# Kernel optimization log

Hardware: AMD Instinct MI355X
Metric: run time of the kernel (lower is better)

## Reference

```python
import jax, jax.numpy as jnp
import numpy as np
import math
from jax import lax

IMG = 1024
STRIDES = (4, 8, 16, 32, 64)
RATIOS = (0.5, 1.0, 2.0)
PRE_NMS = 1000      # pre_nms_top_n['testing'] per level
POST_NMS = 1000     # post_nms_top_n['testing']
NMS_T = 0.7
MIN_SIZE = 1e-3
SCORE_T = 0.0
BBOX_CLAMP = math.log(1000.0 / 16.0)  # torchvision BoxCoder clamp
LEVEL_SIZES = tuple(((IMG // s) ** 2) * len(RATIOS) for s in STRIDES)  # (196608,49152,12288,3072,768)
A_TOTAL = sum(LEVEL_SIZES)
N_IMG = 16


def _make_anchors():
    ratios = np.asarray(RATIOS, dtype=np.float64)
    h_r = np.sqrt(ratios)
    w_r = 1.0 / h_r
    out = []
    for lvl, s in enumerate(STRIDES):
        size = 32.0 * (2 ** lvl)
        ws, hs = w_r * size, h_r * size
        base = np.stack([-ws / 2, -hs / 2, ws / 2, hs / 2], axis=1)  # [A,4]
        g = IMG // s
        coords = np.arange(g, dtype=np.float64) * s
        sx, sy = np.meshgrid(coords, coords)  # [g,g], row = H
        shifts = np.stack([sx, sy, sx, sy], axis=-1).reshape(-1, 1, 4)  # [g*g,1,4] in (H,W,A) order
        out.append((shifts + base[None]).reshape(-1, 4))
    return np.concatenate(out, 0).astype(np.float32)


def setup_inputs() -> dict:
    key = jax.random.key(0)
    k1, k2 = jax.random.split(key)
    objectness = jax.random.normal(k1, (N_IMG, A_TOTAL), dtype=jnp.float32)
    deltas = jax.random.normal(k2, (N_IMG, A_TOTAL, 4), dtype=jnp.float32) * 0.1
    anchors = jnp.asarray(_make_anchors())
    return {"objectness": objectness, "deltas": deltas, "anchors": anchors}


def _decode(deltas, anchors):
    # torchvision BoxCoder.decode with weights (1,1,1,1); deltas [N,A,4], anchors [A,4]
    wa = anchors[:, 2] - anchors[:, 0]
    ha = anchors[:, 3] - anchors[:, 1]
    cxa = anchors[:, 0] + 0.5 * wa
    cya = anchors[:, 1] + 0.5 * ha
    dx, dy, dw, dh = (deltas[..., 0], deltas[..., 1], deltas[..., 2], deltas[..., 3])
    dw = jnp.minimum(dw, BBOX_CLAMP)
    dh = jnp.minimum(dh, BBOX_CLAMP)
    cx = dx * wa + cxa
    cy = dy * ha + cya
    w = jnp.exp(dw) * wa
    h = jnp.exp(dh) * ha
    return jnp.stack([cx - 0.5 * w, cy - 0.5 * h, cx + 0.5 * w, cy + 0.5 * h], axis=-1)


def _nms_image(boxes, scores, lvl, valid):
    # batched_nms via per-level coordinate offset, then greedy NMS over score-sorted boxes.
    max_c = jnp.max(boxes)
    off = lvl.astype(boxes.dtype) * (max_c + 1.0)
    b_off = boxes + off[:, None]
    s = jnp.where(valid, scores, -1.0)
    order = jnp.argsort(-s)
    b = b_off[order]          # [K,4] offset boxes, score-descending
    bo = boxes[order]
    so = scores[order]
    vo = valid[order]
    K = b.shape[0]
    areas = (b[:, 2] - b[:, 0]) * (b[:, 3] - b[:, 1])
    idx = jnp.arange(K)

    def body(keep, xs):
        i, bi, vi = xs
        lt = jnp.maximum(bi[:2], b[:, :2])
        rb = jnp.minimum(bi[2:], b[:, 2:])
        wh = jnp.clip(rb - lt, 0.0)
        inter = wh[:, 0] * wh[:, 1]
        ai = (bi[2] - bi[0]) * (bi[3] - bi[1])
        union = ai + areas - inter
        iou = jnp.where(union > 0, inter / union, 0.0)
        suppressed = jnp.any(keep & (idx < i) & (iou > NMS_T))
        return keep.at[i].set(vi & ~suppressed), None

    keep, _ = lax.scan(body, jnp.zeros((K,), bool), (idx, b, vo))
    # compact kept entries (already score-ordered) into POST_NMS slots, pad with zeros
    pos = jnp.cumsum(keep) - 1
    slot = jnp.where(keep & (pos < POST_NMS), pos, POST_NMS)
    out_b = jnp.zeros((POST_NMS + 1, 4), boxes.dtype).at[slot].set(bo)[:POST_NMS]
    out_s = jnp.zeros((POST_NMS + 1,), boxes.dtype).at[slot].set(so)[:POST_NMS]
    return out_b, out_s


def reference(objectness, deltas, anchors):
    N = objectness.shape[0]
    proposals = _decode(deltas, anchors)  # [N,A,4]
    # per-level top-k (pre-NMS)
    idxs = []
    offset = 0
    for n in LEVEL_SIZES:
        k = min(PRE_NMS, n)
        _, ti = lax.top_k(objectness[:, offset:offset + n], k)
        idxs.append(ti + offset)
        offset += n
    top_idx = jnp.concatenate(idxs, axis=1)  # [N,K]
    obj = jnp.take_along_axis(objectness, top_idx, axis=1)
    props = jnp.take_along_axis(proposals, top_idx[..., None], axis=1)
    lvl_full = jnp.asarray(np.repeat(np.arange(len(LEVEL_SIZES)), LEVEL_SIZES))
    lvl = lvl_full[top_idx]
    scores = jax.nn.sigmoid(obj)
    # clip to image
    x = jnp.clip(props[..., 0::2], 0.0, float(IMG))
    y = jnp.clip(props[..., 1::2], 0.0, float(IMG))
    boxes = jnp.stack([x[..., 0], y[..., 0], x[..., 1], y[..., 1]], axis=-1)
    # remove small boxes + score threshold (as validity mask)
    w = boxes[..., 2] - boxes[..., 0]
    h = boxes[..., 3] - boxes[..., 1]
    valid = (w >= MIN_SIZE) & (h >= MIN_SIZE) & (scores >= SCORE_T)
    out_boxes, out_scores = jax.vmap(_nms_image)(boxes, scores, lvl, valid)
    return out_boxes, out_scores
```

## Files before the change

kernel.cpp:

```cpp
#include <hip/hip_runtime.h>
#include <stdint.h>

#define NIMG 16
#define ATOT 261888
#define TOTC 4768
#define POSTN 1000
#define ROWQ 75
#define EQCAP 8192
#define SCAP 1088
#define BPRE 24
#define DM 0.7000000178813934326171875

__device__ __forceinline__ unsigned sortable_u32(float f) {
  unsigned b = __float_as_uint(f);
  return (b & 0x80000000u) ? ~b : (b | 0x80000000u);
}

__device__ __forceinline__ float exp_xla(float x) {
  float xc = fminf(x, 88.72283935546875f);
  xc = fmaxf(xc, -87.33654022216796875f);
  float n = floorf(fmaf(xc, 1.44269504088896341f, 0.5f));
  float r = fmaf(n, -0.693359375f, xc);
  r = fmaf(n, 2.12194440e-4f, r);
  float y = 1.9875691500e-4f;
  y = fmaf(y, r, 1.3981999507e-3f);
  y = fmaf(y, r, 8.3334519073e-3f);
  y = fmaf(y, r, 4.1665795894e-2f);
  y = fmaf(y, r, 1.6666665459e-1f);
  y = fmaf(y, r, 5.0000001201e-1f);
  float r2 = r * r;
  y = fmaf(y, r2, r);
  y = y + 1.0f;
  return ldexpf(y, (int)n);
}

__device__ __forceinline__ float sigmoid_ref(float x) {
#pragma clang fp contract(off)
  float e = exp_xla(-x);
  return 1.0f / (1.0f + e);
}

__device__ __forceinline__ void chunk_map4k(int c, int& lvl, int& start, int& cnt) {
  if (c < 48)      { lvl = 0; start = c * 4096;        cnt = 4096; }
  else if (c < 60) { lvl = 1; start = (c - 48) * 4096; cnt = 4096; }
  else if (c < 63) { lvl = 2; start = (c - 60) * 4096; cnt = 4096; }
  else             { lvl = 3; start = 0;               cnt = 3072; }
}
__constant__ int d_LO[5] = {0, 196608, 245760, 258048, 261120};
__constant__ int d_CO[5] = {0, 1000, 2000, 3000, 4000};

__global__ void __launch_bounds__(256) k_hist(const float* __restrict__ obj,
                                              unsigned* __restrict__ hist) {
  int img = blockIdx.x >> 6, c = blockIdx.x & 63;
  int lvl, start, cnt;
  chunk_map4k(c, lvl, start, cnt);
  const float4* p4 = (const float4*)(obj + (size_t)img * ATOT + d_LO[lvl] + start);
  __shared__ unsigned h[256];
  h[threadIdx.x] = 0;
  __syncthreads();
  int nv = cnt >> 2;
  for (int i = threadIdx.x; i < nv; i += 256) {
    float4 v = p4[i];
    atomicAdd(&h[sortable_u32(v.x) >> 24], 1u);
    atomicAdd(&h[sortable_u32(v.y) >> 24], 1u);
    atomicAdd(&h[sortable_u32(v.z) >> 24], 1u);
    atomicAdd(&h[sortable_u32(v.w) >> 24], 1u);
  }
  __syncthreads();
  unsigned* gh = hist + (img * 4 + lvl) * 256;
  if (h[threadIdx.x]) atomicAdd(&gh[threadIdx.x], h[threadIdx.x]);
}

__global__ void __launch_bounds__(64) k_thresh(const unsigned* __restrict__ hist,
                                               unsigned* __restrict__ thr) {
  int il = blockIdx.x;
  if (threadIdx.x != 0) return;
  const unsigned* h = hist + il * 256;
  unsigned krem = 1000, cum = 0;
  int d = 255;
  for (; d > 0; --d) {
    if (cum + h[d] >= krem) break;
    cum += h[d];
  }
  thr[il * 2] = (unsigned)d;
  thr[il * 2 + 1] = krem - cum;
}

__global__ void __launch_bounds__(256) k_emit(const float* __restrict__ obj,
                                              const unsigned* __restrict__ thr,
                                              int* __restrict__ cand,
                                              int* __restrict__ eqbuf,
                                              unsigned* __restrict__ cnt) {
  int img = blockIdx.x / 65, c = blockIdx.x % 65;
  if (c == 64) {
    for (int i = threadIdx.x; i < 768; i += 256)
      cand[img * TOTC + d_CO[4] + i] = d_LO[4] + i;
    return;
  }
  int lvl, start, cntn;
  chunk_map4k(c, lvl, start, cntn);
  int il = img * 4 + lvl;
  unsigned d0 = thr[il * 2];
  int gbase = d_LO[lvl] + start;
  const float4* p4 = (const float4*)(obj + (size_t)img * ATOT + gbase);
  int nv = cntn >> 2;
  int cbase = img * TOTC + d_CO[lvl];

  __shared__ int gts[SCAP], eqs[SCAP];
  __shared__ int nGt, nEq, gtBase, eqBase;
  if (threadIdx.x == 0) { nGt = 0; nEq = 0; }
  __syncthreads();

  float4 v[4];
  int ni = 0;
#pragma unroll
  for (int k = 0; k < 4; ++k) {
    int i = threadIdx.x + k * 256;
    if (i < nv) { v[k] = p4[i]; ni = k + 1; }
  }
#pragma unroll
  for (int k = 0; k < 4; ++k) {
    if (k >= ni) break;
    float vv[4] = {v[k].x, v[k].y, v[k].z, v[k].w};
#pragma unroll
    for (int c4 = 0; c4 < 4; ++c4) {
      unsigned u = sortable_u32(vv[c4]);
      unsigned d = u >> 24;
      if (d >= d0) {
        int gidx = gbase + (threadIdx.x + k * 256) * 4 + c4;
        if (d > d0) {
          int p = atomicAdd(&nGt, 1);
          if (p < SCAP) gts[p] = gidx;
          else { int s = (int)atomicAdd(&cnt[il * 2], 1u); cand[cbase + s] = gidx; }
        } else {
          int p = atomicAdd(&nEq, 1);
          if (p < SCAP) eqs[p] = gidx;
          else { int e = (int)atomicAdd(&cnt[il * 2 + 1], 1u); if (e < EQCAP) eqbuf[il * EQCAP + e] = gidx; }
        }
      }
    }
  }
  __syncthreads();
  int ng = nGt < SCAP ? nGt : SCAP;
  int ne = nEq < SCAP ? nEq : SCAP;
  if (threadIdx.x == 0) {
    gtBase = (int)atomicAdd(&cnt[il * 2], (unsigned)ng);
    eqBase = (int)atomicAdd(&cnt[il * 2 + 1], (unsigned)ne);
  }
  __syncthreads();
  for (int k = threadIdx.x; k < ng; k += 256) cand[cbase + gtBase + k] = gts[k];
  for (int k = threadIdx.x; k < ne; k += 256) {
    int e = eqBase + k;
    if (e < EQCAP) eqbuf[il * EQCAP + e] = eqs[k];
  }
}

__global__ void __launch_bounds__(256) k_refine(const float* __restrict__ obj,
                                                const unsigned* __restrict__ thr,
                                                const int* __restrict__ eqbuf,
                                                const unsigned* __restrict__ cnt,
                                                int* __restrict__ cand) {
  int il = blockIdx.x;
  int img = il >> 2, lvl = il & 3;
  unsigned pref = thr[il * 2];
  unsigned krem = thr[il * 2 + 1];
  int neq = min((int)cnt[il * 2 + 1], EQCAP);
  int cgt = (int)cnt[il * 2];
  const float* p = obj + (size_t)img * ATOT;
  const int* eq = eqbuf + il * EQCAP;
  int cbase = img * TOTC + d_CO[lvl];
  __shared__ unsigned h[256];
  __shared__ unsigned s_pref, s_krem;
  for (int round = 1; round < 4; ++round) {
    int shift = 24 - 8 * round;
    h[threadIdx.x] = 0;
    __syncthreads();
    for (int e = threadIdx.x; e < neq; e += 256) {
      unsigned u = sortable_u32(p[eq[e]]);
      if ((u >> (shift + 8)) == pref) atomicAdd(&h[(u >> shift) & 255u], 1u);
    }
    __syncthreads();
    if (threadIdx.x == 0) {
      unsigned cum = 0;
      int d = 255;
      for (; d > 0; --d) {
        if (cum + h[d] >= krem) break;
        cum += h[d];
      }
      s_pref = (pref << 8) | (unsigned)d;
      s_krem = krem - cum;
    }
    __syncthreads();
    pref = s_pref;
    krem = s_krem;
    __syncthreads();
  }
  __shared__ int cg2, ce2;
  __shared__ int eqi[1024];
  if (threadIdx.x == 0) { cg2 = 0; ce2 = 0; }
  __syncthreads();
  for (int e = threadIdx.x; e < neq; e += 256) {
    int gidx = eq[e];
    unsigned u = sortable_u32(p[gidx]);
    if (u > pref) {
      int s = atomicAdd(&cg2, 1);
      cand[cbase + cgt + s] = gidx;
    } else if (u == pref) {
      int s2 = atomicAdd(&ce2, 1);
      if (s2 < 1024) eqi[s2] = gidx;
    }
  }
  __syncthreads();
  if (threadIdx.x == 0) {
    int ne = ce2 < 1024 ? ce2 : 1024;
    int base = cgt + cg2;
    for (int r = 0; r < (int)krem; ++r) {
      int besti = -1, bestv = 0x7fffffff;
      for (int e2 = 0; e2 < ne; ++e2) {
        int v = eqi[e2];
        if (v >= 0 && v < bestv) { bestv = v; besti = e2; }
      }
      if (besti < 0) break;
      eqi[besti] = -1;
      cand[cbase + base + r] = bestv;
    }
  }
}

__global__ void __launch_bounds__(1024) k_lvlsort(const float* __restrict__ obj,
                                                  int* __restrict__ cand) {
  const int KL[5] = {1000, 1000, 1000, 1000, 768};
  const int CO[5] = {0, 1000, 2000, 3000, 4000};
  int img = blockIdx.x / 5, lvl = blockIdx.x % 5;
  int k = KL[lvl];
  int cbase = img * TOTC + CO[lvl];
  int tid = threadIdx.x;
  __shared__ unsigned long long sh[1024];
  unsigned long long key = 0ull;
  if (tid < k) {
    int idx = cand[cbase + tid];
    unsigned u = sortable_u32(obj[(size_t)img * ATOT + idx]);
    key = ((unsigned long long)u << 32) | (unsigned)(0xFFFFFFFFu - (unsigned)idx);
  }
  sh[tid] = key;
  __syncthreads();
  for (int kk = 2; kk <= 1024; kk <<= 1)
    for (int j = kk >> 1; j > 0; j >>= 1) {
      int ixj = tid ^ j;
      if (ixj > tid) {
        unsigned long long a = sh[tid], b = sh[ixj];
        bool up2 = ((tid & kk) == 0);
        if ((a < b) == up2) { sh[tid] = b; sh[ixj] = a; }
      }
      __syncthreads();
    }
  if (tid < k) {
    unsigned low = (unsigned)(sh[tid] & 0xFFFFFFFFull);
    cand[cbase + tid] = (int)(0xFFFFFFFFu - low);
  }
}

__global__ void __launch_bounds__(256) k_decode(const float* __restrict__ obj,
                                                const float* __restrict__ del,
                                                const float* __restrict__ anc,
                                                const int* __restrict__ cand,
                                                float* __restrict__ boxo,
                                                float* __restrict__ keyf,
                                                unsigned* __restrict__ skey,
                                                unsigned* __restrict__ maxcb) {
#pragma clang fp contract(off)
  int img = blockIdx.x;
  int c = blockIdx.y * 256 + threadIdx.x;
  float m = 0.0f;
  if (c < TOTC) {
    int a = cand[img * TOTC + c];
    float o = obj[(size_t)img * ATOT + a];
    float s = sigmoid_ref(o);
    const float* ap = anc + (size_t)a * 4;
    float a0 = ap[0], a1 = ap[1], a2 = ap[2], a3 = ap[3];
    const float* dp = del + ((size_t)img * ATOT + (size_t)a) * 4;
    float dx = dp[0], dy = dp[1], dw = dp[2], dh = dp[3];
    float wa = a2 - a0, ha = a3 - a1;
    float cxa = a0 + 0.5f * wa, cya = a1 + 0.5f * ha;
    dw = fminf(dw, 4.135166556742356f);
    dh = fminf(dh, 4.135166556742356f);
    float cx = dx * wa + cxa;
    float cy = dy * ha + cya;
    float w = exp_xla(dw) * wa;
    float h = exp_xla(dh) * ha;
    float x1 = cx - 0.5f * w, y1 = cy - 0.5f * h;
    float x2 = cx + 0.5f * w, y2 = cy + 0.5f * h;
    x1 = fminf(fmaxf(x1, 0.0f), 1024.0f);
    x2 = fminf(fmaxf(x2, 0.0f), 1024.0f);
    y1 = fminf(fmaxf(y1, 0.0f), 1024.0f);
    y2 = fminf(fmaxf(y2, 0.0f), 1024.0f);
    float ww = x2 - x1, hh = y2 - y1;
    bool valid = (ww >= 1e-3f) && (hh >= 1e-3f) && (s >= 0.0f);
    float kf = valid ? s : -1.0f;
    float4 bx = make_float4(x1, y1, x2, y2);
    *(float4*)(boxo + (size_t)(img * TOTC + c) * 4) = bx;
    keyf[img * TOTC + c] = kf;
    skey[img * TOTC + c] = sortable_u32(kf);
    m = fmaxf(fmaxf(x1, x2), fmaxf(y1, y2));
  }
  __shared__ float red[256];
  red[threadIdx.x] = m;
  __syncthreads();
  for (int s2 = 128; s2 > 0; s2 >>= 1) {
    if (threadIdx.x < s2) red[threadIdx.x] = fmaxf(red[threadIdx.x], red[threadIdx.x + s2]);
    __syncthreads();
  }
  if (threadIdx.x == 0) atomicMax(&maxcb[img], __float_as_uint(red[0]));
}

__global__ void __launch_bounds__(256) k_rank(const unsigned* __restrict__ skey,
                                              int* __restrict__ ord) {
  int img = blockIdx.x / 19;
  int tile = blockIdx.x % 19;
  __shared__ unsigned long long keys[TOTC];
  const unsigned* sk = skey + img * TOTC;
  for (int k = threadIdx.x; k < TOTC; k += 256)
    keys[k] = ((unsigned long long)sk[k] << 16) | (unsigned)(0xFFFF - k);
  __syncthreads();
  int i = tile * 256 + threadIdx.x;
  if (i >= TOTC) return;
  unsigned long long my = keys[i];
  int cnt = 0;
  int j = 0;
  for (; j + 8 <= TOTC; j += 8) {
#pragma unroll
    for (int u = 0; u < 8; ++u) cnt += (keys[j + u] > my) ? 1 : 0;
  }
  for (; j < TOTC; ++j) cnt += (keys[j] > my) ? 1 : 0;
  ord[img * TOTC + cnt] = i;
}

__global__ void __launch_bounds__(256) k_srec(const float* __restrict__ boxo,
                                              const float* __restrict__ keyf,
                                              const int* __restrict__ ord,
                                              const unsigned* __restrict__ maxcb,
                                              float* __restrict__ srec,
                                              int* __restrict__ rinv,
                                              unsigned long long* __restrict__ validw) {
#pragma clang fp contract(off)
  int img = blockIdx.x;
  int i = blockIdx.y * 256 + threadIdx.x;
  if (i >= TOTC) return;
  int p = ord[img * TOTC + i];
  int lvl = p / 1000;
  if (lvl > 4) lvl = 4;
  float4 b = *(const float4*)(boxo + (size_t)(img * TOTC + p) * 4);
  float maxc = __uint_as_float(maxcb[img]);
  float off = (float)lvl * (maxc + 1.0f);
  float ox1 = b.x + off, oy1 = b.y + off, ox2 = b.z + off, oy2 = b.w + off;
  float area = (ox2 - ox1) * (oy2 - oy1);
  float kf = keyf[img * TOTC + p];
  float* r = srec + (size_t)(img * TOTC + i) * 12;
  r[0] = ox1; r[1] = oy1; r[2] = ox2; r[3] = oy2;
  r[4] = area; r[5] = kf;
  r[6] = b.x; r[7] = b.y; r[8] = b.z; r[9] = b.w;
  r[10] = __int_as_float(lvl); r[11] = 0.0f;
  rinv[img * TOTC + p] = i;
  bool valid = kf > -0.5f;
  unsigned long long vb = __ballot(valid);
  if ((threadIdx.x & 63) == 0 && (i >> 6) < ROWQ) validw[img * ROWQ + (i >> 6)] = vb;
}

__global__ void __launch_bounds__(256) k_iou(const float* __restrict__ srec,
                                             unsigned long long* __restrict__ mat) {
#pragma clang fp contract(off)
  int gb = blockIdx.x;
  int img = gb / 21;
  int g = gb % 21;
  int t, jcg;
  if (g < 6)       { t = 0; jcg = g; }
  else if (g < 11) { t = 1; jcg = g - 6; }
  else if (g < 15) { t = 2; jcg = g - 11; }
  else if (g < 18) { t = 3; jcg = g - 15; }
  else if (g < 20) { t = 4; jcg = g - 18; }
  else             { t = 5; jcg = g - 20; }
  int jcbase = (t + jcg) * 4;

  const int tid = threadIdx.x;
  const int i = t * 256 + tid;
  const float* sb = srec + (size_t)img * TOTC * 12;

  __shared__ float4 s_box[256];
  __shared__ float s_area[256];
  {
    int j = jcbase * 64 + tid;
    const float* r = sb + (size_t)j * 12;
    s_box[tid] = *(const float4*)r;
    s_area[tid] = r[4];
  }

  const float* rr = sb + (size_t)i * 12;
  float4 bb = *(const float4*)rr;
  float ix1 = bb.x, iy1 = bb.y, ix2 = bb.z, iy2 = bb.w;
  float ia = rr[4];
  __syncthreads();

  unsigned long long* rowp = mat + ((size_t)img * TOTC + (size_t)i) * ROWQ;
#pragma unroll
  for (int kk = 0; kk < 4; ++kk) {
    int jc = jcbase + kk;
    unsigned long long bits = 0ull;
    for (int b = 0; b < 64; ++b) {
      float4 jb = s_box[kk * 64 + b];
      float ja = s_area[kk * 64 + b];
      float ltx = fmaxf(ix1, jb.x), lty = fmaxf(iy1, jb.y);
      float rbx = fminf(ix2, jb.z), rby = fminf(iy2, jb.w);
      float w = fmaxf(rbx - ltx, 0.0f), h = fmaxf(rby - lty, 0.0f);
      float inter = w * h;
      float uni = (ia + ja) - inter;
      bool sup = (uni > 0.0f) && ((double)inter >= DM * (double)uni);
      if (sup) bits |= (1ull << b);
    }
    rowp[jc] = bits;
  }
}

__global__ void __launch_bounds__(512) k_resolve(const unsigned long long* __restrict__ mat,
                                                 const unsigned long long* __restrict__ validw,
                                                 const float* __restrict__ srec,
                                                 float* __restrict__ out) {
  const int img = blockIdx.x;
  const int tid = threadIdx.x;
  const int lane = tid & 63;
  const int wid = tid >> 6;
  const unsigned long long* matb = mat + (size_t)img * TOTC * ROWQ;
  const float* sb = srec + (size_t)img * TOTC * 12;
  float* ob = out + (size_t)img * POSTN * 4;
  float* os = out + (size_t)NIMG * POSTN * 4 + (size_t)img * POSTN;

  __shared__ int alist[1088];
  __shared__ unsigned long long vw[BPRE];
  __shared__ unsigned long long part[2][8];
  __shared__ unsigned long long sh_keep;
  __shared__ int sh_nacc;
  __shared__ float kb[POSTN][5];

  for (int t = tid; t < BPRE; t += 512) vw[t] = validw[img * ROWQ + t];

  unsigned long long s0 = 0ull;
  int nacc = 0;

  unsigned long long diagcur = 0ull;
  if (wid == 0) diagcur = matb[(size_t)lane * ROWQ + 0];
  __syncthreads();

  for (int B = 0; B < BPRE; ++B) {
    if (lane == B) part[B & 1][wid] = s0;
    __syncthreads();

    unsigned long long supB = part[B & 1][0] | part[B & 1][1] | part[B & 1][2] | part[B & 1][3] |
                              part[B & 1][4] | part[B & 1][5] | part[B & 1][6] | part[B & 1][7];
    unsigned long long alive = vw[B] & ~supB;
    const int ibase = B * 64;

    unsigned long long m = alive;
    for (int t = 0; t < wid; ++t) if (m) m &= m - 1ull;
    auto popi = [&]() -> int {
      if (!m) return -1;
      int b = __builtin_ctzll(m);
      m &= m - 1ull;
#pragma unroll
      for (int t = 0; t < 7; ++t) if (m) m &= m - 1ull;
      return ibase + b;
    };
    int i0 = popi(), i1 = popi(), i2 = popi(), i3 = popi();
    int i4 = popi(), i5 = popi(), i6 = popi(), i7 = popi();
    unsigned long long r0 = 0, r1 = 0, r2 = 0, r3 = 0, r4 = 0, r5 = 0, r6 = 0, r7 = 0;
    bool lok = lane < BPRE;
    if (i0 >= 0 && lok) r0 = matb[(size_t)i0 * ROWQ + lane];
    if (i1 >= 0 && lok) r1 = matb[(size_t)i1 * ROWQ + lane];
    if (i2 >= 0 && lok) r2 = matb[(size_t)i2 * ROWQ + lane];
    if (i3 >= 0 && lok) r3 = matb[(size_t)i3 * ROWQ + lane];
    if (i4 >= 0 && lok) r4 = matb[(size_t)i4 * ROWQ + lane];
    if (i5 >= 0 && lok) r5 = matb[(size_t)i5 * ROWQ + lane];
    if (i6 >= 0 && lok) r6 = matb[(size_t)i6 * ROWQ + lane];
    if (i7 >= 0 && lok) r7 = matb[(size_t)i7 * ROWQ + lane];

    unsigned long long diagnext = 0ull;
    if (wid == 0) {
      int ibn = (B + 1) * 64 + lane;
      if (B + 1 < BPRE) diagnext = matb[(size_t)ibn * ROWQ + (B + 1)];
      bool alv = ((alive >> lane) & 1ull) != 0ull;
      unsigned long long rem = alive, keepm = 0ull;
      while (rem) {
        int b = __builtin_ctzll(rem);
        keepm |= (1ull << b);
        bool sup = ((diagcur >> b) & 1ull) != 0ull;
        alv = alv && !sup;
        unsigned long long nb = __ballot(alv);
        rem = (b < 63) ? (nb & (~0ull << (b + 1))) : 0ull;
      }
      if (lane == 0) sh_keep = keepm;
      if ((keepm >> lane) & 1ull) {
        int pos = nacc + __popcll(keepm & ((1ull << lane) - 1ull));
        alist[pos] = ibase + lane;
      }
    }
    __syncthreads();
    unsigned long long keepm = sh_keep;
    nacc += __popcll(keepm);
    if (nacc >= POSTN) break;

    if (i0 >= 0 && ((keepm >> (i0 - ibase)) & 1ull)) s0 |= r0;
    if (i1 >= 0 && ((keepm >> (i1 - ibase)) & 1ull)) s0 |= r1;
    if (i2 >= 0 && ((keepm >> (i2 - ibase)) & 1ull)) s0 |= r2;
    if (i3 >= 0 && ((keepm >> (i3 - ibase)) & 1ull)) s0 |= r3;
    if (i4 >= 0 && ((keepm >> (i4 - ibase)) & 1ull)) s0 |= r4;
    if (i5 >= 0 && ((keepm >> (i5 - ibase)) & 1ull)) s0 |= r5;
    if (i6 >= 0 && ((keepm >> (i6 - ibase)) & 1ull)) s0 |= r6;
    if (i7 >= 0 && ((keepm >> (i7 - ibase)) & 1ull)) s0 |= r7;
    if (wid == 0) diagcur = diagnext;
  }

  if (nacc < POSTN) {
    for (int k = tid; k < nacc; k += 512) {
      const float* rec = sb + (size_t)alist[k] * 12;
      kb[k][0] = rec[0]; kb[k][1] = rec[1]; kb[k][2] = rec[2]; kb[k][3] = rec[3]; kb[k][4] = rec[4];
    }
    __syncthreads();
    if (wid == 0) {
      int n = nacc;
      for (int r = BPRE * 64; r < TOTC && n < POSTN; ++r) {
        const float* rec = sb + (size_t)r * 12;
        float4 bx = *(const float4*)rec;
        float ra = rec[4];
        float kf = rec[5];
        bool sup = false;
        for (int j = lane; j < n; j += 64) {
          float ltx = fmaxf(bx.x, kb[j][0]), lty = fmaxf(bx.y, kb[j][1]);
          float rbx = fminf(bx.z, kb[j][2]), rby = fminf(bx.w, kb[j][3]);
          float w = fmaxf(rbx - ltx, 0.0f), h = fmaxf(rby - lty, 0.0f);
          float inter = w * h;
          float uni = (ra + kb[j][4]) - inter;
          if (uni > 0.0f && (double)inter >= DM * (double)uni) sup = true;
        }
        bool any = (__ballot(sup) != 0ull);
        if (kf > -0.5f && !any) {
          if (lane == 0) {
            alist[n] = r;
            kb[n][0] = bx.x; kb[n][1] = bx.y; kb[n][2] = bx.z; kb[n][3] = bx.w; kb[n][4] = ra;
          }
          asm volatile("s_waitcnt lgkmcnt(0)" ::: "memory");
          ++n;
        }
      }
      if (lane == 0) sh_nacc = n;
    }
    __syncthreads();
    nacc = sh_nacc;
  }

  __syncthreads();
  int nout = nacc < POSTN ? nacc : POSTN;
  for (int k = tid; k < nout; k += 512) {
    int i = alist[k];
    const float* rec = sb + (size_t)i * 12;
    ob[(size_t)k * 4 + 0] = rec[6];
    ob[(size_t)k * 4 + 1] = rec[7];
    ob[(size_t)k * 4 + 2] = rec[8];
    ob[(size_t)k * 4 + 3] = rec[9];
    os[k] = rec[5];
  }
}

extern "C" void kernel_launch(void* const* d_in, const int* in_sizes, int n_in,
                              void* d_out, int out_size, void* d_ws, size_t ws_size,
                              hipStream_t stream) {
  const float* obj = (const float*)d_in[0];
  const float* del = (const float*)d_in[1];
  const float* anc = (const float*)d_in[2];
  float* out = (float*)d_out;

  char* w = (char*)d_ws;
  size_t o = 0;
  auto carve = [&](size_t bytes) -> char* {
    char* p = w + o;
    o = (o + bytes + 255) & ~(size_t)255;
    return p;
  };
  int* cand = (int*)carve((size_t)NIMG * TOTC * 4);
  unsigned* skey = (unsigned*)carve((size_t)NIMG * TOTC * 4);
  float* keyf = (float*)carve((size_t)NIMG * TOTC * 4);
  int* ord = (int*)carve((size_t)NIMG * TOTC * 4);
  int* rinv = (int*)carve((size_t)NIMG * TOTC * 4);
  float* boxo = (float*)carve((size_t)NIMG * TOTC * 16);
  float* srec = (float*)carve((size_t)NIMG * TOTC * 48);
  unsigned* maxcb = (unsigned*)carve(64);
  unsigned* hist = (unsigned*)carve((size_t)64 * 256 * 4);
  unsigned* thr = (unsigned*)carve((size_t)64 * 2 * 4);
  unsigned* cnt = (unsigned*)carve((size_t)64 * 2 * 4);
  int* eqbuf = (int*)carve((size_t)64 * EQCAP * 4);
  unsigned long long* validw = (unsigned long long*)carve((size_t)NIMG * ROWQ * 8);
  unsigned long long* mat = (unsigned long long*)carve((size_t)NIMG * TOTC * ROWQ * 8);

  hipMemsetAsync(d_out, 0, (size_t)out_size * sizeof(float), stream);
  hipMemsetAsync(maxcb, 0, 16 * sizeof(unsigned), stream);
  hipMemsetAsync(hist, 0, (size_t)64 * 256 * 4, stream);
  hipMemsetAsync(cnt, 0, (size_t)64 * 2 * 4, stream);

  k_hist<<<16 * 64, 256, 0, stream>>>(obj, hist);
  k_thresh<<<64, 64, 0, stream>>>(hist, thr);
  k_emit<<<16 * 65, 256, 0, stream>>>(obj, thr, cand, eqbuf, cnt);
  k_refine<<<64, 256, 0, stream>>>(obj, thr, eqbuf, cnt, cand);
  k_lvlsort<<<80, 1024, 0, stream>>>(obj, cand);
  k_decode<<<dim3(16, (TOTC + 255) / 256), 256, 0, stream>>>(obj, del, anc, cand, boxo, keyf, skey, maxcb);
  k_rank<<<16 * 19, 256, 0, stream>>>(skey, ord);
  k_srec<<<dim3(16, (TOTC + 255) / 256), 256, 0, stream>>>(boxo, keyf, ord, maxcb, srec, rinv, validw);
  k_iou<<<16 * 21, 256, 0, stream>>>(srec, mat);
  k_resolve<<<16, 512, 0, stream>>>(mat, validw, srec, out);
}
```

Baseline: 318.7 us.

## Replace level bitonic sort with rank sort and fuse scatter into rank kernel

The per-level bitonic sort (1024 threads, many barriers) becomes a counting-rank sort over shared memory keys with 256 threads. The global rank kernel now scatters sorted records straight into srec, which removes the separate k_srec kernel along with the ord and rinv buffers. The valid-bit ballot moves into k_iou. This cuts one launch and one global round trip, but the rank sort costs O(k^2) comparisons per level and the srec writes become scattered.

Measured after the change: 368.5 us. +15.6%, slower.

```diff
diff --git a/kernel.cpp b/kernel.cpp
--- a/kernel.cpp
+++ b/kernel.cpp
@@ -227,36 +227,32 @@
   }
 }
 
-__global__ void __launch_bounds__(1024) k_lvlsort(const float* __restrict__ obj,
-                                                  int* __restrict__ cand) {
+__global__ void __launch_bounds__(256) k_lrank(const float* __restrict__ obj,
+                                               int* __restrict__ cand) {
   const int KL[5] = {1000, 1000, 1000, 1000, 768};
   const int CO[5] = {0, 1000, 2000, 3000, 4000};
   int img = blockIdx.x / 5, lvl = blockIdx.x % 5;
   int k = KL[lvl];
   int cbase = img * TOTC + CO[lvl];
-  int tid = threadIdx.x;
-  __shared__ unsigned long long sh[1024];
-  unsigned long long key = 0ull;
-  if (tid < k) {
-    int idx = cand[cbase + tid];
+  __shared__ unsigned long long keys[1000];
+  __shared__ int idxs[1000];
+  for (int t = threadIdx.x; t < k; t += 256) {
+    int idx = cand[cbase + t];
     unsigned u = sortable_u32(obj[(size_t)img * ATOT + idx]);
-    key = ((unsigned long long)u << 32) | (unsigned)(0xFFFFFFFFu - (unsigned)idx);
-  }
-  sh[tid] = key;
-  __syncthreads();
-  for (int kk = 2; kk <= 1024; kk <<= 1)
-    for (int j = kk >> 1; j > 0; j >>= 1) {
-      int ixj = tid ^ j;
-      if (ixj > tid) {
-        unsigned long long a = sh[tid], b = sh[ixj];
-        bool up2 = ((tid & kk) == 0);
-        if ((a < b) == up2) { sh[tid] = b; sh[ixj] = a; }
-      }
-      __syncthreads();
-    }
-  if (tid < k) {
-    unsigned low = (unsigned)(sh[tid] & 0xFFFFFFFFull);
-    cand[cbase + tid] = (int)(0xFFFFFFFFu - low);
+    keys[t] = ((unsigned long long)u << 32) | (unsigned)(0xFFFFFFFFu - (unsigned)idx);
+    idxs[t] = idx;
+  }
+  __syncthreads();
+  for (int t = threadIdx.x; t < k; t += 256) {
+    unsigned long long my = keys[t];
+    int cnt = 0;
+    int j = 0;
+    for (; j + 8 <= k; j += 8) {
+#pragma unroll
+      for (int u = 0; u < 8; ++u) cnt += (keys[j + u] > my) ? 1 : 0;
+    }
+    for (; j < k; ++j) cnt += (keys[j] > my) ? 1 : 0;
+    cand[cbase + cnt] = idxs[t];
   }
 }
 
@@ -314,7 +310,11 @@
 }
 
 __global__ void __launch_bounds__(256) k_rank(const unsigned* __restrict__ skey,
-                                              int* __restrict__ ord) {
+                                              const float* __restrict__ boxo,
+                                              const float* __restrict__ keyf,
+                                              const unsigned* __restrict__ maxcb,
+                                              float* __restrict__ srec) {
+#pragma clang fp contract(off)
   int img = blockIdx.x / 19;
   int tile = blockIdx.x % 19;
   __shared__ unsigned long long keys[TOTC];
@@ -332,21 +332,7 @@
     for (int u = 0; u < 8; ++u) cnt += (keys[j + u] > my) ? 1 : 0;
   }
   for (; j < TOTC; ++j) cnt += (keys[j] > my) ? 1 : 0;
-  ord[img * TOTC + cnt] = i;
-}
-
-__global__ void __launch_bounds__(256) k_srec(const float* __restrict__ boxo,
-                                              const float* __restrict__ keyf,
-                                              const int* __restrict__ ord,
-                                              const unsigned* __restrict__ maxcb,
-                                              float* __restrict__ srec,
-                                              int* __restrict__ rinv,
-                                              unsigned long long* __restrict__ validw) {
-#pragma clang fp contract(off)
-  int img = blockIdx.x;
-  int i = blockIdx.y * 256 + threadIdx.x;
-  if (i >= TOTC) return;
-  int p = ord[img * TOTC + i];
+  int p = i;
   int lvl = p / 1000;
   if (lvl > 4) lvl = 4;
   float4 b = *(const float4*)(boxo + (size_t)(img * TOTC + p) * 4);
@@ -355,19 +341,16 @@
   float ox1 = b.x + off, oy1 = b.y + off, ox2 = b.z + off, oy2 = b.w + off;
   float area = (ox2 - ox1) * (oy2 - oy1);
   float kf = keyf[img * TOTC + p];
-  float* r = srec + (size_t)(img * TOTC + i) * 12;
+  float* r = srec + (size_t)(img * TOTC + cnt) * 12;
   r[0] = ox1; r[1] = oy1; r[2] = ox2; r[3] = oy2;
   r[4] = area; r[5] = kf;
   r[6] = b.x; r[7] = b.y; r[8] = b.z; r[9] = b.w;
   r[10] = __int_as_float(lvl); r[11] = 0.0f;
-  rinv[img * TOTC + p] = i;
-  bool valid = kf > -0.5f;
-  unsigned long long vb = __ballot(valid);
-  if ((threadIdx.x & 63) == 0 && (i >> 6) < ROWQ) validw[img * ROWQ + (i >> 6)] = vb;
 }
 
 __global__ void __launch_bounds__(256) k_iou(const float* __restrict__ srec,
-                                             unsigned long long* __restrict__ mat) {
+                                             unsigned long long* __restrict__ mat,
+                                             unsigned long long* __restrict__ validw) {
 #pragma clang fp contract(off)
   int gb = blockIdx.x;
   int img = gb / 21;
@@ -398,6 +381,11 @@
   float4 bb = *(const float4*)rr;
   float ix1 = bb.x, iy1 = bb.y, ix2 = bb.z, iy2 = bb.w;
   float ia = rr[4];
+  if (jcg == 0) {
+    bool valid = rr[5] > -0.5f;
+    unsigned long long vb = __ballot(valid);
+    if ((tid & 63) == 0) validw[img * ROWQ + (i >> 6)] = vb;
+  }
   __syncthreads();
 
   unsigned long long* rowp = mat + ((size_t)img * TOTC + (size_t)i) * ROWQ;
@@ -586,8 +574,6 @@
   int* cand = (int*)carve((size_t)NIMG * TOTC * 4);
   unsigned* skey = (unsigned*)carve((size_t)NIMG * TOTC * 4);
   float* keyf = (float*)carve((size_t)NIMG * TOTC * 4);
-  int* ord = (int*)carve((size_t)NIMG * TOTC * 4);
-  int* rinv = (int*)carve((size_t)NIMG * TOTC * 4);
   float* boxo = (float*)carve((size_t)NIMG * TOTC * 16);
   float* srec = (float*)carve((size_t)NIMG * TOTC * 48);
   unsigned* maxcb = (unsigned*)carve(64);
@@ -607,10 +593,9 @@
   k_thresh<<<64, 64, 0, stream>>>(hist, thr);
   k_emit<<<16 * 65, 256, 0, stream>>>(obj, thr, cand, eqbuf, cnt);
   k_refine<<<64, 256, 0, stream>>>(obj, thr, eqbuf, cnt, cand);
-  k_lvlsort<<<80, 1024, 0, stream>>>(obj, cand);
+  k_lrank<<<80, 256, 0, stream>>>(obj, cand);
   k_decode<<<dim3(16, (TOTC + 255) / 256), 256, 0, stream>>>(obj, del, anc, cand, boxo, keyf, skey, maxcb);
-  k_rank<<<16 * 19, 256, 0, stream>>>(skey, ord);
-  k_srec<<<dim3(16, (TOTC + 255) / 256), 256, 0, stream>>>(boxo, keyf, ord, maxcb, srec, rinv, validw);
-  k_iou<<<16 * 21, 256, 0, stream>>>(srec, mat);
+  k_rank<<<16 * 19, 256, 0, stream>>>(skey, boxo, keyf, maxcb, srec);
+  k_iou<<<16 * 21, 256, 0, stream>>>(srec, mat, validw);
   k_resolve<<<16, 512, 0, stream>>>(mat, validw, srec, out);
 }
```
